# Kernel optimization log

Hardware: AMD Instinct MI355X
Metric: run time of the kernel (lower is better)

The kernel has to match this reference:

```python
import jax, jax.numpy as jnp
import numpy as np

V0 = 25; WIN = 3; NS = 6; EPS = 1e-5

def _build_scales():
    # ring graph on 25 joints (matches A_binary in init_kwargs)
    A = np.zeros((V0, V0), np.float32)
    for i in range(V0):
        A[i, (i + 1) % V0] = 1.0; A[(i + 1) % V0, i] = 1.0
    AL = np.tile(A + np.eye(V0, dtype=A.dtype), (WIN, WIN))  # spatial-temporal graph (75x75)
    I = np.eye(len(AL), dtype=AL.dtype)
    def shell(k):
        return np.minimum(np.linalg.matrix_power(AL + I, k), 1) - np.minimum(np.linalg.matrix_power(AL + I, k - 1), 1)
    def kadj(k):
        return I.copy() if k == 0 else shell(k) + I  # with_self=True
    def norm(g):
        dinv = np.power(g.sum(-1), -0.5)
        Dm = np.eye(len(g)) * dinv
        return (Dm @ g @ Dm).astype(np.float32)
    def klap(k):
        if k == 0:
            return I.astype(np.float32)
        Ak = shell(k)
        D = Ak.sum(-1)
        Dm = np.eye(len(D)) * np.power(D, -0.5)
        return (Dm @ (np.eye(len(D)) * (D + 2) - Ak) @ Dm).astype(np.float32)
    A_scales = np.concatenate([norm(kadj(k)) for k in range(NS)])  # (NS*75, 75)
    B_scales = np.concatenate([klap(k) for k in range(NS)])        # (NS*75, 75)
    return jnp.asarray(A_scales), jnp.asarray(B_scales)

def _bn(x, g, b):
    # BatchNorm2d in training mode: batch stats over (N, T, V)
    m = x.mean(axis=(0, 2, 3), keepdims=True)
    v = x.var(axis=(0, 2, 3), keepdims=True)
    return (x - m) * jax.lax.rsqrt(v + EPS) * g[None, :, None, None] + b[None, :, None, None]

def setup_inputs():
    key = jax.random.key(0)
    ks = jax.random.split(key, 4)
    N, C, T = 8, 96, 128
    A_scales, B_scales = _build_scales()
    d_in = C * NS * 2
    return {
        'x': jax.random.normal(ks[0], (N, C, T, V0), jnp.float32),
        'A_scales': A_scales,
        'B_scales': B_scales,
        'A_res': jax.random.uniform(ks[1], A_scales.shape, jnp.float32, -1e-6, 1e-6),
        'W_mlp': jax.random.normal(ks[2], (C, d_in), jnp.float32) / np.sqrt(d_in),
        'b_mlp': jnp.zeros((C,), jnp.float32),
        'g1': jnp.ones((C,), jnp.float32),
        'bt1': jnp.zeros((C,), jnp.float32),
        'W_out': jax.random.normal(ks[3], (C, C, WIN), jnp.float32) / np.sqrt(C * WIN),
        'b_out': jnp.zeros((C,), jnp.float32),
        'g2': jnp.ones((C,), jnp.float32),
        'bt2': jnp.zeros((C,), jnp.float32),
    }

def _forward(x, A_scales, B_scales, A_res, W_mlp, b_mlp, g1, bt1, W_out, b_out, g2, bt2):
    N, C, T, V = x.shape
    xp = jnp.pad(x, ((0, 0), (0, 0), (1, 1), (0, 0)))
    xu = jnp.stack([xp[:, :, w:w + T, :] for w in range(WIN)], axis=3).reshape(N, C, T, WIN * V)
    VL = WIN * V
    A = A_scales + A_res
    B = B_scales + A_res
    def agg(M):
        a = jnp.einsum('vu,nctu->nctv', M, xu)               # (N, C, T, NS*VL)
        a = a.reshape(N, C, T, NS, VL).transpose(0, 3, 1, 2, 4)
        return a.reshape(N, NS * C, T, VL)
    h = jnp.concatenate([agg(A), agg(B)], axis=1)            # (N, 2*NS*C, T, VL)
    # MLP: 1x1 conv -> ReLU -> BN
    h = jnp.einsum('oi,nitv->notv', W_mlp, h) + b_mlp[None, :, None, None]
    h = _bn(jax.nn.relu(h), g1, bt1)
    h = jax.nn.relu(h)                                       # gcn: act(mlp + residual(=0))
    h = h.reshape(N, C, T, WIN, V)
    out = jnp.einsum('oiw,nitwv->notv', W_out, h) + b_out[None, :, None, None]
    return _bn(out, g2, bt2)

def reference(x, A_scales, B_scales, A_res, W_mlp, b_mlp, g1, bt1, W_out, b_out, g2, bt2):
    return _forward(x, A_scales, B_scales, A_res, W_mlp, b_mlp, g1, bt1, W_out, b_out, g2, bt2)
```

## Files before the change

kernel.cpp:

```cpp
#include <hip/hip_runtime.h>


#define NB 8
#define CB 96
#define TB 128
#define VB 25
#define VLB 75
#define EPSB 1e-5f
#define XRS 104
#define TMS 104
#define HBS 296

typedef __attribute__((ext_vector_type(8))) short bf16x8;
typedef __attribute__((ext_vector_type(4))) float f32x4;

__device__ inline unsigned short f2bf(float f) {
  unsigned int u = __float_as_uint(f);
  u = (u + 0x7FFFu + ((u >> 16) & 1u)) >> 16;
  return (unsigned short)u;
}
__device__ inline float bf2f(unsigned short u) {
  return __uint_as_float(((unsigned int)u) << 16);
}

__global__ __launch_bounds__(256) void k0_init(
    const float* __restrict__ As, const float* __restrict__ Bs,
    const float* __restrict__ Ar, const float* __restrict__ Wm,
    const float* __restrict__ Wo,
    unsigned short* __restrict__ ABsw, unsigned short* __restrict__ Wsw,
    unsigned short* __restrict__ Wosw, float* __restrict__ stats) {
  int i = blockIdx.x * 256 + threadIdx.x;
  if (i < 110592) {
    int ps = i / 9216, r = i % 9216;
    int wv = r / 1536, r2 = r % 1536;
    int kk = r2 / 512, r3 = r2 % 512;
    int lane = r3 / 8, j = r3 % 8;
    int o = wv * 16 + (lane & 15);
    int c = kk * 32 + (lane >> 4) * 8 + j;
    Wsw[i] = f2bf(Wm[o * 1152 + ps * 96 + c]);
  }
  if (i < 92160) {
    int ps = i / 7680, r = i % 7680;
    int nt = r / 1536, r2 = r % 1536;
    int kk = r2 / 512, r3 = r2 % 512;
    int lane = r3 / 8, j = r3 % 8;
    int u = nt * 16 + (lane & 15);
    int up = kk * 32 + (lane >> 4) * 8 + j;
    float v = 0.f;
    if (u < 75 && up < 75) {
      int path = ps / 6, s = ps % 6;
      int idx = (s * 75 + u) * 75 + up;
      v = (path == 0 ? As[idx] : Bs[idx]) + Ar[idx];
    }
    ABsw[i] = f2bf(v);
  }
  if (i < 27648) {
    int wv = i / 4608, r = i % 4608;
    int kk = r / 512, r3 = r % 512;
    int lane = r3 / 8, j = r3 % 8;
    int o = wv * 16 + (lane & 15);
    int k = kk * 32 + (lane >> 4) * 8 + j;
    Wosw[i] = f2bf(Wo[o * 288 + k]);
  }
  if (i < 384) stats[i] = 0.f;
}

__global__ __launch_bounds__(384, 2) void k1t2(
    const float* __restrict__ x, const unsigned short* __restrict__ ABsw,
    const unsigned short* __restrict__ Wsw, const float* __restrict__ bm,
    unsigned short* __restrict__ h_relu, float* __restrict__ stats1) {
  __shared__ unsigned short xraw[112 * XRS];
  __shared__ unsigned short tmp_s[2][96 * TMS];
  __shared__ float st1s[96], st2s[96];
  const int tid = threadIdx.x;
  const int n = blockIdx.x >> 6, t0 = (blockIdx.x & 63) * 2;
  const int wave = tid >> 6, lane = tid & 63;
  const int l15 = lane & 15, quad = lane >> 4, q8 = quad * 8;
  const int wrow16 = wave * 16;

  for (int idx = tid; idx < 96 * 112; idx += 384) {
    int c = idx / 112, r = idx - c * 112;
    float v = 0.f;
    if (r < 100) {
      int tt = t0 - 1 + r / 25, vv = r % 25;
      if (tt >= 0 && tt < TB) v = x[((n * CB + c) * TB + tt) * VB + vv];
    }
    xraw[r * XRS + c] = f2bf(v);
  }
  for (int idx = tid; idx < 2 * 96 * 16; idx += 384) {
    int b = idx / (96 * 16), rem = idx - b * 96 * 16;
    tmp_s[b][(rem / 16) * TMS + 80 + rem % 16] = 0;
  }
  __syncthreads();

  const f32x4 zf = {0.f, 0.f, 0.f, 0.f};
  f32x4 acc2[2][5];
#pragma unroll
  for (int d = 0; d < 2; ++d)
#pragma unroll
    for (int nt = 0; nt < 5; ++nt) acc2[d][nt] = zf;

  const unsigned short* Wbase = Wsw + wave * 1536 + lane * 8;
  const unsigned short* Bbase = ABsw + lane * 8;

#pragma unroll
  for (int ps = 0; ps < 12; ++ps) {
    bf16x8 wa[3];
#pragma unroll
    for (int kk = 0; kk < 3; ++kk)
      wa[kk] = *reinterpret_cast<const bf16x8*>(Wbase + ps * 9216 + kk * 512);
    bf16x8 bf[15];
#pragma unroll
    for (int i = 0; i < 15; ++i)
      bf[i] = *reinterpret_cast<const bf16x8*>(Bbase + ps * 7680 + i * 512);

    f32x4 acc1[5];
#pragma unroll
    for (int nt = 0; nt < 5; ++nt) acc1[nt] = zf;
#pragma unroll
    for (int kk = 0; kk < 3; ++kk)
#pragma unroll
      for (int nt = 0; nt < 5; ++nt) {
        bf16x8 b = *reinterpret_cast<const bf16x8*>(&xraw[(nt * 16 + l15) * XRS + kk * 32 + q8]);
        acc1[nt] = __builtin_amdgcn_mfma_f32_16x16x32_bf16(wa[kk], b, acc1[nt], 0, 0, 0);
      }
#pragma unroll
    for (int nt = 0; nt < 5; ++nt) {
      int col = nt * 16 + l15;
#pragma unroll
      for (int r = 0; r < 4; ++r) {
        unsigned short v = (col < 75) ? f2bf(acc1[nt][r]) : (unsigned short)0;
        tmp_s[0][(wrow16 + quad * 4 + r) * TMS + col] = v;
      }
    }
#pragma unroll
    for (int nt = 0; nt < 5; ++nt) acc1[nt] = zf;
#pragma unroll
    for (int kk = 0; kk < 3; ++kk)
#pragma unroll
      for (int nt = 0; nt < 5; ++nt) {
        bf16x8 b = *reinterpret_cast<const bf16x8*>(&xraw[(25 + nt * 16 + l15) * XRS + kk * 32 + q8]);
        acc1[nt] = __builtin_amdgcn_mfma_f32_16x16x32_bf16(wa[kk], b, acc1[nt], 0, 0, 0);
      }
#pragma unroll
    for (int nt = 0; nt < 5; ++nt) {
      int col = nt * 16 + l15;
#pragma unroll
      for (int r = 0; r < 4; ++r) {
        unsigned short v = (col < 75) ? f2bf(acc1[nt][r]) : (unsigned short)0;
        tmp_s[1][(wrow16 + quad * 4 + r) * TMS + col] = v;
      }
    }

#pragma unroll
    for (int kk = 0; kk < 3; ++kk) {
      bf16x8 a0 = *reinterpret_cast<const bf16x8*>(&tmp_s[0][(wrow16 + l15) * TMS + kk * 32 + q8]);
#pragma unroll
      for (int nt = 0; nt < 5; ++nt)
        acc2[0][nt] = __builtin_amdgcn_mfma_f32_16x16x32_bf16(a0, bf[nt * 3 + kk], acc2[0][nt], 0, 0, 0);
      bf16x8 a1 = *reinterpret_cast<const bf16x8*>(&tmp_s[1][(wrow16 + l15) * TMS + kk * 32 + q8]);
#pragma unroll
      for (int nt = 0; nt < 5; ++nt)
        acc2[1][nt] = __builtin_amdgcn_mfma_f32_16x16x32_bf16(a1, bf[nt * 3 + kk], acc2[1][nt], 0, 0, 0);
    }
  }

  const int orow = wrow16 + quad * 4;
  float s1[4] = {0.f, 0.f, 0.f, 0.f}, s2[4] = {0.f, 0.f, 0.f, 0.f};
#pragma unroll
  for (int d = 0; d < 2; ++d) {
    const int t = t0 + d;
#pragma unroll
    for (int r = 0; r < 4; ++r) {
      const int o = orow + r;
      const float bias = bm[o];
      unsigned short* hp = h_relu + ((n * CB + o) * TB + t) * VLB;
#pragma unroll
      for (int nt = 0; nt < 5; ++nt) {
        int u = nt * 16 + l15;
        if (u < VLB) {
          float v = acc2[d][nt][r] + bias;
          v = v > 0.f ? v : 0.f;
          hp[u] = f2bf(v);
          s1[r] += v;
          s2[r] += v * v;
        }
      }
    }
  }
#pragma unroll
  for (int off = 1; off < 16; off <<= 1) {
#pragma unroll
    for (int r = 0; r < 4; ++r) {
      s1[r] += __shfl_xor(s1[r], off, 64);
      s2[r] += __shfl_xor(s2[r], off, 64);
    }
  }
  if (l15 == 0) {
#pragma unroll
    for (int r = 0; r < 4; ++r) { st1s[orow + r] = s1[r]; st2s[orow + r] = s2[r]; }
  }
  __syncthreads();
  if (tid < 96) {
    atomicAdd(&stats1[tid], st1s[tid]);
    atomicAdd(&stats1[96 + tid], st2s[tid]);
  }
}

__global__ __launch_bounds__(384) void k3n(
    const unsigned short* __restrict__ h_relu, const float* __restrict__ stats1,
    const float* __restrict__ g1, const float* __restrict__ bt1,
    const unsigned short* __restrict__ Wosw, const float* __restrict__ bo,
    float* __restrict__ out_pre, float* __restrict__ stats2) {
  __shared__ unsigned short hnb[2][32 * HBS];
  __shared__ float a1s[96], b1s[96];
  __shared__ float st1[96], st2[96];
  const int tid = threadIdx.x;
  const int n = blockIdx.x >> 6, t0 = (blockIdx.x & 63) * 2;

  if (tid < 96) {
    const float inv = 1.f / (8.f * 128.f * 75.f);
    float m = stats1[tid] * inv;
    float var = stats1[96 + tid] * inv - m * m;
    float a = g1[tid] * rsqrtf(var + EPSB);
    a1s[tid] = a;
    b1s[tid] = bt1[tid] - m * a;
  }
  for (int idx = tid; idx < 2 * 7 * HBS; idx += 384) {
    int d = idx / (7 * HBS), rm = idx % (7 * HBS);
    hnb[d][25 * HBS + rm] = 0;
  }
  __syncthreads();

  for (int idx = tid; idx < 2 * 96 * 75; idx += 384) {
    int d = idx / 7200, rm = idx % 7200;
    int i = rm / 75, u = rm - i * 75;
    float hv = bf2f(h_relu[((n * CB + i) * TB + t0 + d) * VLB + u]);
    float v = a1s[i] * hv + b1s[i];
    v = v > 0.f ? v : 0.f;
    int w = u / 25, vv = u - w * 25;
    hnb[d][vv * HBS + i * 3 + w] = f2bf(v);
  }
  __syncthreads();

  const int wave = tid >> 6, lane = tid & 63;
  const int l15 = lane & 15, quad = lane >> 4, q8 = quad * 8;
  const f32x4 zf = {0.f, 0.f, 0.f, 0.f};
  f32x4 acc[2][2] = {{zf, zf}, {zf, zf}};
  const unsigned short* Apw = Wosw + wave * 4608 + lane * 8;
#pragma unroll
  for (int kk = 0; kk < 9; ++kk) {
    bf16x8 a = *reinterpret_cast<const bf16x8*>(Apw + kk * 512);
#pragma unroll
    for (int d = 0; d < 2; ++d) {
      bf16x8 b0 = *reinterpret_cast<const bf16x8*>(&hnb[d][l15 * HBS + kk * 32 + q8]);
      bf16x8 b1 = *reinterpret_cast<const bf16x8*>(&hnb[d][(16 + l15) * HBS + kk * 32 + q8]);
      acc[d][0] = __builtin_amdgcn_mfma_f32_16x16x32_bf16(a, b0, acc[d][0], 0, 0, 0);
      acc[d][1] = __builtin_amdgcn_mfma_f32_16x16x32_bf16(a, b1, acc[d][1], 0, 0, 0);
    }
  }

  const int orow = wave * 16 + quad * 4;
  float s1[4] = {0.f, 0.f, 0.f, 0.f}, s2[4] = {0.f, 0.f, 0.f, 0.f};
#pragma unroll
  for (int d = 0; d < 2; ++d) {
#pragma unroll
    for (int nt = 0; nt < 2; ++nt) {
      int v = nt * 16 + l15;
      if (v < VB) {
#pragma unroll
        for (int r = 0; r < 4; ++r) {
          const int o = orow + r;
          float val = acc[d][nt][r] + bo[o];
          out_pre[((n * CB + o) * TB + t0 + d) * VB + v] = val;
          s1[r] += val;
          s2[r] += val * val;
        }
      }
    }
  }
#pragma unroll
  for (int off = 1; off < 16; off <<= 1) {
#pragma unroll
    for (int r = 0; r < 4; ++r) {
      s1[r] += __shfl_xor(s1[r], off, 64);
      s2[r] += __shfl_xor(s2[r], off, 64);
    }
  }
  if (l15 == 0) {
#pragma unroll
    for (int r = 0; r < 4; ++r) { st1[orow + r] = s1[r]; st2[orow + r] = s2[r]; }
  }
  __syncthreads();
  if (tid < 96) {
    atomicAdd(&stats2[tid], st1[tid]);
    atomicAdd(&stats2[96 + tid], st2[tid]);
  }
}

__global__ __launch_bounds__(256) void k5_bn2(
    const float* __restrict__ out_pre, const float* __restrict__ stats2,
    const float* __restrict__ g2, const float* __restrict__ bt2,
    float* __restrict__ out) {
  int idx = blockIdx.x * 256 + threadIdx.x;
  if (idx >= NB * CB * TB * VB / 4) return;
  int o = (idx / (TB * VB / 4)) % CB;
  const float inv = 1.f / (8.f * 128.f * 25.f);
  float m = stats2[o] * inv;
  float var = stats2[96 + o] * inv - m * m;
  float a = g2[o] * rsqrtf(var + EPSB);
  float b = bt2[o] - m * a;
  f32x4 vin = reinterpret_cast<const f32x4*>(out_pre)[idx];
  f32x4 vo;
#pragma unroll
  for (int j = 0; j < 4; ++j) vo[j] = a * vin[j] + b;
  reinterpret_cast<f32x4*>(out)[idx] = vo;
}

extern "C" void kernel_launch(void* const* d_in, const int* in_sizes, int n_in,
                              void* d_out, int out_size, void* d_ws, size_t ws_size,
                              hipStream_t stream) {
  const float* x   = (const float*)d_in[0];
  const float* As  = (const float*)d_in[1];
  const float* Bs  = (const float*)d_in[2];
  const float* Ar  = (const float*)d_in[3];
  const float* Wm  = (const float*)d_in[4];
  const float* bm  = (const float*)d_in[5];
  const float* g1  = (const float*)d_in[6];
  const float* bt1 = (const float*)d_in[7];
  const float* Wo  = (const float*)d_in[8];
  const float* bo  = (const float*)d_in[9];
  const float* g2  = (const float*)d_in[10];
  const float* bt2 = (const float*)d_in[11];
  float* out = (float*)d_out;

  char* base = (char*)d_ws;
  unsigned short* HR   = (unsigned short*)base;
  float* out_pre       = (float*)(base + 14745600);
  unsigned short* ABsw = (unsigned short*)(base + 24576000);
  unsigned short* Wsw  = (unsigned short*)(base + 24760320);
  unsigned short* Wosw = (unsigned short*)(base + 24981504);
  float* stats         = (float*)(base + 25036800);
  float* stats1 = stats, *stats2 = stats + 192;

  k0_init<<<432, 256, 0, stream>>>(As, Bs, Ar, Wm, Wo, ABsw, Wsw, Wosw, stats);
  k1t2<<<NB * TB / 2, 384, 0, stream>>>(x, ABsw, Wsw, bm, HR, stats1);
  k3n<<<NB * TB / 2, 384, 0, stream>>>(HR, stats1, g1, bt1, Wosw, bo, out_pre, stats2);
  k5_bn2<<<(NB * CB * TB * VB / 4 + 255) / 256, 256, 0, stream>>>(out_pre, stats2, g2, bt2, out);
}
```

Measured before the change: 191.2 us.

## Make h_relu time-major for vectorized loads and move BN2 stats to separate kernel

```diff
diff --git a/kernel.cpp b/kernel.cpp
--- a/kernel.cpp
+++ b/kernel.cpp
@@ -174,7 +174,7 @@
     for (int r = 0; r < 4; ++r) {
       const int o = orow + r;
       const float bias = bm[o];
-      unsigned short* hp = h_relu + ((n * CB + o) * TB + t) * VLB;
+      unsigned short* hp = h_relu + ((n * TB + t) * CB + o) * VLB;
 #pragma unroll
       for (int nt = 0; nt < 5; ++nt) {
         int u = nt * 16 + l15;
@@ -211,10 +211,9 @@
     const unsigned short* __restrict__ h_relu, const float* __restrict__ stats1,
     const float* __restrict__ g1, const float* __restrict__ bt1,
     const unsigned short* __restrict__ Wosw, const float* __restrict__ bo,
-    float* __restrict__ out_pre, float* __restrict__ stats2) {
+    float* __restrict__ out_pre) {
   __shared__ unsigned short hnb[2][32 * HBS];
   __shared__ float a1s[96], b1s[96];
-  __shared__ float st1[96], st2[96];
   const int tid = threadIdx.x;
   const int n = blockIdx.x >> 6, t0 = (blockIdx.x & 63) * 2;
 
@@ -232,14 +231,21 @@
   }
   __syncthreads();
 
-  for (int idx = tid; idx < 2 * 96 * 75; idx += 384) {
-    int d = idx / 7200, rm = idx % 7200;
-    int i = rm / 75, u = rm - i * 75;
-    float hv = bf2f(h_relu[((n * CB + i) * TB + t0 + d) * VLB + u]);
-    float v = a1s[i] * hv + b1s[i];
-    v = v > 0.f ? v : 0.f;
-    int w = u / 25, vv = u - w * 25;
-    hnb[d][vv * HBS + i * 3 + w] = f2bf(v);
+  const unsigned short* hp = h_relu + (n * TB + t0) * (CB * VLB);
+  for (int i8 = tid; i8 < 1800; i8 += 384) {
+    bf16x8 v = *reinterpret_cast<const bf16x8*>(hp + i8 * 8);
+    int ee = i8 * 8;
+    int d = (ee >= 7200) ? 1 : 0;
+    int rem = ee - d * 7200;
+#pragma unroll
+    for (int j = 0; j < 8; ++j) {
+      int e = rem + j;
+      int i = e / 75, u = e - i * 75;
+      float val = a1s[i] * bf2f((unsigned short)v[j]) + b1s[i];
+      val = val > 0.f ? val : 0.f;
+      int w = u / 25, vv = u - w * 25;
+      hnb[d][vv * HBS + i * 3 + w] = f2bf(val);
+    }
   }
   __syncthreads();
 
@@ -261,7 +267,6 @@
   }
 
   const int orow = wave * 16 + quad * 4;
-  float s1[4] = {0.f, 0.f, 0.f, 0.f}, s2[4] = {0.f, 0.f, 0.f, 0.f};
 #pragma unroll
   for (int d = 0; d < 2; ++d) {
 #pragma unroll
@@ -271,30 +276,42 @@
 #pragma unroll
         for (int r = 0; r < 4; ++r) {
           const int o = orow + r;
-          float val = acc[d][nt][r] + bo[o];
-          out_pre[((n * CB + o) * TB + t0 + d) * VB + v] = val;
-          s1[r] += val;
-          s2[r] += val * val;
+          out_pre[((n * CB + o) * TB + t0 + d) * VB + v] = acc[d][nt][r] + bo[o];
         }
       }
     }
   }
-#pragma unroll
-  for (int off = 1; off < 16; off <<= 1) {
-#pragma unroll
-    for (int r = 0; r < 4; ++r) {
-      s1[r] += __shfl_xor(s1[r], off, 64);
-      s2[r] += __shfl_xor(s2[r], off, 64);
-    }
-  }
-  if (l15 == 0) {
-#pragma unroll
-    for (int r = 0; r < 4; ++r) { st1[orow + r] = s1[r]; st2[orow + r] = s2[r]; }
-  }
-  __syncthreads();
-  if (tid < 96) {
-    atomicAdd(&stats2[tid], st1[tid]);
-    atomicAdd(&stats2[96 + tid], st2[tid]);
+}
+
+__global__ __launch_bounds__(256) void k4_stats(
+    const float* __restrict__ out_pre, float* __restrict__ stats2) {
+  __shared__ float ws1[4], ws2[4];
+  const int tid = threadIdx.x;
+  const int o = blockIdx.x % CB, p = blockIdx.x / CB;
+  float s1 = 0.f, s2 = 0.f;
+#pragma unroll
+  for (int k = 0; k < 2; ++k) {
+    const int n = 2 * p + k;
+    const f32x4* base = reinterpret_cast<const f32x4*>(out_pre + (n * CB + o) * (TB * VB));
+    for (int idx = tid; idx < TB * VB / 4; idx += 256) {
+      f32x4 v = base[idx];
+#pragma unroll
+      for (int j = 0; j < 4; ++j) { s1 += v[j]; s2 += v[j] * v[j]; }
+    }
+  }
+#pragma unroll
+  for (int off = 1; off < 64; off <<= 1) {
+    s1 += __shfl_xor(s1, off, 64);
+    s2 += __shfl_xor(s2, off, 64);
+  }
+  const int wave = tid >> 6;
+  if ((tid & 63) == 0) { ws1[wave] = s1; ws2[wave] = s2; }
+  __syncthreads();
+  if (tid == 0) {
+    float r1 = ws1[0] + ws1[1] + ws1[2] + ws1[3];
+    float r2 = ws2[0] + ws2[1] + ws2[2] + ws2[3];
+    atomicAdd(&stats2[o], r1);
+    atomicAdd(&stats2[96 + o], r2);
   }
 }
 
@@ -345,6 +362,7 @@
 
   k0_init<<<432, 256, 0, stream>>>(As, Bs, Ar, Wm, Wo, ABsw, Wsw, Wosw, stats);
   k1t2<<<NB * TB / 2, 384, 0, stream>>>(x, ABsw, Wsw, bm, HR, stats1);
-  k3n<<<NB * TB / 2, 384, 0, stream>>>(HR, stats1, g1, bt1, Wosw, bo, out_pre, stats2);
+  k3n<<<NB * TB / 2, 384, 0, stream>>>(HR, stats1, g1, bt1, Wosw, bo, out_pre);
+  k4_stats<<<CB * 4, 256, 0, stream>>>(out_pre, stats2);
   k5_bn2<<<(NB * CB * TB * VB / 4 + 255) / 256, 256, 0, stream>>>(out_pre, stats2, g2, bt2, out);
 }
```

Measured after the change: 182.7 us. 1.05x faster.
